# Kernel optimization log

Hardware: AMD Instinct MI355X
Metric: run time of the kernel (lower is better)

Reference implementation:

```python
import jax, jax.numpy as jnp
import numpy as np

N = 8192      # nodes
D_IN = 128    # input features
D_H = 48      # GAT hidden (hardcoded in module)
D_OUT = 32    # control output dim
NEG_INF = -9e15  # matches torch code's -9000000000000000.0


def setup_inputs() -> dict:
    key = jax.random.key(0)
    ks = jax.random.split(key, 12)
    s = 0.05
    return {
        "x": jax.random.normal(ks[0], (N, D_IN), jnp.float32),
        "adj": jax.random.randint(ks[1], (N, N), 0, 2, jnp.int32),
        "W_gat": jax.random.normal(ks[2], (D_H, D_IN), jnp.float32) * s,
        "a": jax.random.normal(ks[3], (1, D_H), jnp.float32) * s,
        "gamma": jnp.ones((D_H,), jnp.float32),
        "beta": jnp.zeros((D_H,), jnp.float32),
        "W1": jax.random.normal(ks[4], (256, D_H), jnp.float32) * s,
        "b1": jnp.zeros((256,), jnp.float32),
        "W2": jax.random.normal(ks[5], (128, 256), jnp.float32) * s,
        "b2": jnp.zeros((128,), jnp.float32),
        "W3": jax.random.normal(ks[6], (D_OUT, 128), jnp.float32) * s,
        "b3": jnp.zeros((D_OUT,), jnp.float32),
    }


def reference(x, adj, W_gat, a, gamma, beta, W1, b1, W2, b2, W3, b3):
    # --- LightweightGATLayer ---
    Wh = x @ W_gat.T                      # [N, D_H]
    s = Wh @ a.T                          # [N, 1] additive attention scores
    e = s + s.T                           # [N, N]
    e = jnp.where(e > 0, e, 0.2 * e)      # LeakyReLU(0.2)
    e = jnp.where(adj > 0, e, NEG_INF)    # mask non-edges
    attn = jax.nn.softmax(e, axis=1)      # row softmax; dropout is identity in eval
    h_prime = attn @ Wh                   # [N, D_H]
    # LayerNorm over last dim, eps=1e-5
    mu = jnp.mean(h_prime, axis=-1, keepdims=True)
    var = jnp.var(h_prime, axis=-1, keepdims=True)
    h = (h_prime - mu) * jax.lax.rsqrt(var + 1e-5) * gamma + beta
    # --- BiACT MLP head: 48 -> 256 -> 128 -> D_OUT ---
    h = jax.nn.relu(h @ W1.T + b1)
    h = jax.nn.relu(h @ W2.T + b2)
    return h @ W3.T + b3                  # [N, D_OUT]
```

## Files before the change

### kernel.cpp

```cpp
#include <hip/hip_runtime.h>

#define N 8192
#define DIN 128
#define DH 48
#define MT 256
#define KC 64
#define PSTR (KC + 8)
#define NSPLIT 16
#define JSPAN (N / NSPLIT)
#define NCHUNK (JSPAN / KC)
#define ACC_STRIDE 64
#define RB 32

typedef _Float16 half8 __attribute__((ext_vector_type(8)));
typedef float f32x4 __attribute__((ext_vector_type(4)));

__global__ __launch_bounds__(256) void k_wh(const float* __restrict__ x,
                                            const float* __restrict__ Wg,
                                            float* __restrict__ Wh) {
    __shared__ float wT[DIN * DH];
    int t = threadIdx.x;
    for (int e = t; e < DIN * DH; e += 256) {
        int c = e / DIN, k = e % DIN;
        wT[k * DH + c] = Wg[e];
    }
    __syncthreads();
    int o = blockIdx.x * 256 + t;
    int r = o / DH, c = o % DH;
    const float4* xr = (const float4*)(x + (size_t)r * DIN);
    float acc = 0.f;
    #pragma unroll 8
    for (int k4 = 0; k4 < DIN / 4; ++k4) {
        float4 xv = xr[k4];
        int kb = k4 * 4;
        acc += xv.x * wT[(kb + 0) * DH + c];
        acc += xv.y * wT[(kb + 1) * DH + c];
        acc += xv.z * wT[(kb + 2) * DH + c];
        acc += xv.w * wT[(kb + 3) * DH + c];
    }
    Wh[o] = acc;
}

__global__ __launch_bounds__(256) void k_s(const float* __restrict__ Wh,
                                           const float* __restrict__ a,
                                           float* __restrict__ s) {
    int r = blockIdx.x * 256 + threadIdx.x;
    const float4* wr = (const float4*)(Wh + (size_t)r * DH);
    const float4* av = (const float4*)a;
    float acc = 0.f;
    #pragma unroll
    for (int k4 = 0; k4 < DH / 4; ++k4) {
        float4 w = wr[k4]; float4 aa = av[k4];
        acc += w.x * aa.x + w.y * aa.y + w.z * aa.z + w.w * aa.w;
    }
    s[r] = acc;
}

__global__ __launch_bounds__(256) void k_gat(const int* __restrict__ adj,
                                             const float* __restrict__ Wh,
                                             const float* __restrict__ s,
                                             float* __restrict__ accWs) {
    __shared__ _Float16 pS[MT][PSTR];
    __shared__ _Float16 wS[64][PSTR];
    __shared__ float sRow[MT];
    int t = threadIdx.x;
    int tile = blockIdx.x & 31;
    int split = blockIdx.x >> 5;
    int i0 = tile * MT;
    int jbase = split * JSPAN;

    sRow[t] = s[i0 + t];
    for (int e = t; e < 16 * PSTR; e += 256) {
        int n = 48 + e / PSTR, k = e % PSTR;
        wS[n][k] = (n == 48) ? (_Float16)1.0f : (_Float16)0.0f;
    }

    int lane = t & 63, w = t >> 6;
    int ln16 = lane & 15, kq = lane >> 4;
    int jp = t & 31, rg = t >> 5;

    f32x4 acc[4][4];
    #pragma unroll
    for (int a0 = 0; a0 < 4; ++a0)
        #pragma unroll
        for (int b0 = 0; b0 < 4; ++b0) acc[a0][b0] = (f32x4){0.f, 0.f, 0.f, 0.f};

    __syncthreads();

    for (int chunk = 0; chunk < NCHUNK; ++chunk) {
        int j0 = jbase + chunk * KC;
        #pragma unroll
        for (int k = 0; k < 12; ++k) {
            int e = t + k * 256;
            int jc = e / DH, d = e % DH;
            wS[d][jc] = (_Float16)Wh[(size_t)j0 * DH + e];
        }
        {
            float2 sj = *(const float2*)(s + j0 + 2 * jp);
            #pragma unroll 8
            for (int it = 0; it < 32; ++it) {
                int r = rg * 32 + it;
                int2 av = *(const int2*)(adj + (size_t)(i0 + r) * N + j0 + 2 * jp);
                float e0 = sRow[r] + sj.x;
                float e1 = sRow[r] + sj.y;
                e0 = fmaxf(e0, 0.2f * e0);
                e1 = fmaxf(e1, 0.2f * e1);
                float p0 = av.x ? __expf(e0) : 0.f;
                float p1 = av.y ? __expf(e1) : 0.f;
                union { _Float16 h[2]; unsigned u; } pk;
                pk.h[0] = (_Float16)p0;
                pk.h[1] = (_Float16)p1;
                *(unsigned*)&pS[r][2 * jp] = pk.u;
            }
        }
        __syncthreads();
        {
            const int m0 = w * 64;
            #pragma unroll
            for (int kt = 0; kt < 2; ++kt) {
                const int kk = kt * 32 + kq * 8;
                half8 b[4];
                #pragma unroll
                for (int nt = 0; nt < 4; ++nt)
                    b[nt] = *(const half8*)&wS[nt * 16 + ln16][kk];
                #pragma unroll
                for (int mtl = 0; mtl < 4; ++mtl) {
                    half8 a = *(const half8*)&pS[m0 + mtl * 16 + ln16][kk];
                    #pragma unroll
                    for (int nt = 0; nt < 4; ++nt)
                        acc[mtl][nt] = __builtin_amdgcn_mfma_f32_16x16x32_f16(
                            a, b[nt], acc[mtl][nt], 0, 0, 0);
                }
            }
        }
        __syncthreads();
    }
    size_t rbase = (size_t)split * N + i0;
    #pragma unroll
    for (int mtl = 0; mtl < 4; ++mtl) {
        #pragma unroll
        for (int nt = 0; nt < 4; ++nt) {
            int col = nt * 16 + ln16;
            if (nt == 3 && ln16 != 0) continue;
            #pragma unroll
            for (int reg = 0; reg < 4; ++reg) {
                int row = w * 64 + mtl * 16 + kq * 4 + reg;
                accWs[(rbase + row) * ACC_STRIDE + col] = acc[mtl][nt][reg];
            }
        }
    }
}

__global__ __launch_bounds__(256) void k_mlp(const float* __restrict__ accWs,
                                             const float* __restrict__ gamma,
                                             const float* __restrict__ beta,
                                             const float* __restrict__ W1, const float* __restrict__ b1,
                                             const float* __restrict__ W2, const float* __restrict__ b2,
                                             const float* __restrict__ W3, const float* __restrict__ b3,
                                             float* __restrict__ out) {
    __shared__ float hacc[RB * 49];
    __shared__ float hN[RB * DH];
    __shared__ float h1[RB * 256];
    __shared__ float h2[RB * 128];
    int t = threadIdx.x;
    int r0 = blockIdx.x * RB;

    for (int e = t; e < RB * 49; e += 256) {
        int r = e / 49, d = e % 49;
        size_t base = (size_t)(r0 + r) * ACC_STRIDE + d;
        float v = 0.f;
        #pragma unroll
        for (int sp = 0; sp < NSPLIT; ++sp)
            v += accWs[(size_t)sp * N * ACC_STRIDE + base];
        hacc[r * 49 + d] = v;
    }
    __syncthreads();

    if (t < RB) {
        float invl = 1.f / hacc[t * 49 + 48];
        float sum = 0.f;
        for (int d = 0; d < DH; ++d) sum += hacc[t * 49 + d];
        float mean = sum * invl * (1.f / DH);
        float var = 0.f;
        for (int d = 0; d < DH; ++d) {
            float dv = hacc[t * 49 + d] * invl - mean;
            var += dv * dv;
        }
        var *= (1.f / DH);
        float rs = rsqrtf(var + 1e-5f);
        for (int d = 0; d < DH; ++d) {
            float hv = (hacc[t * 49 + d] * invl - mean) * rs;
            hN[t * DH + d] = hv * gamma[d] + beta[d];
        }
    }
    __syncthreads();

    {
        int c = t;
        float4 wreg[12];
        const float4* wrow = (const float4*)(W1 + c * DH);
        #pragma unroll
        for (int k4 = 0; k4 < 12; ++k4) wreg[k4] = wrow[k4];
        float bias = b1[c];
        for (int r = 0; r < RB; ++r) {
            float acc = bias;
            const float4* hv4 = (const float4*)&hN[r * DH];
            #pragma unroll
            for (int k4 = 0; k4 < 12; ++k4) {
                float4 hv = hv4[k4];
                acc += hv.x * wreg[k4].x + hv.y * wreg[k4].y
                     + hv.z * wreg[k4].z + hv.w * wreg[k4].w;
            }
            h1[r * 256 + c] = fmaxf(acc, 0.f);
        }
    }
    __syncthreads();

    {
        int c = t & 127;
        int g = t >> 7;
        int rb = g * 16;
        float acc[16];
        float bias = b2[c];
        #pragma unroll
        for (int r = 0; r < 16; ++r) acc[r] = bias;
        const float4* wrow = (const float4*)(W2 + c * 256);
        for (int k4 = 0; k4 < 64; ++k4) {
            float4 wv = wrow[k4];
            #pragma unroll
            for (int r = 0; r < 16; ++r) {
                const float4 hv = *(const float4*)(&h1[(rb + r) * 256 + k4 * 4]);
                acc[r] += wv.x * hv.x + wv.y * hv.y + wv.z * hv.z + wv.w * hv.w;
            }
        }
        #pragma unroll
        for (int r = 0; r < 16; ++r)
            h2[(rb + r) * 128 + c] = fmaxf(acc[r], 0.f);
    }
    __syncthreads();

    {
        int c = t & 31;
        int g = t >> 5;
        int rb = g * 4;
        float acc[4];
        float bias = b3[c];
        #pragma unroll
        for (int r = 0; r < 4; ++r) acc[r] = bias;
        const float4* wrow = (const float4*)(W3 + c * 128);
        for (int k4 = 0; k4 < 32; ++k4) {
            float4 wv = wrow[k4];
            #pragma unroll
            for (int r = 0; r < 4; ++r) {
                const float4 hv = *(const float4*)(&h2[(rb + r) * 128 + k4 * 4]);
                acc[r] += wv.x * hv.x + wv.y * hv.y + wv.z * hv.z + wv.w * hv.w;
            }
        }
        #pragma unroll
        for (int r = 0; r < 4; ++r)
            out[(size_t)(r0 + rb + r) * 32 + c] = acc[r];
    }
}

extern "C" void kernel_launch(void* const* d_in, const int* in_sizes, int n_in,
                              void* d_out, int out_size, void* d_ws, size_t ws_size,
                              hipStream_t stream) {
    const float* x     = (const float*)d_in[0];
    const int*   adj   = (const int*)d_in[1];
    const float* Wg    = (const float*)d_in[2];
    const float* a     = (const float*)d_in[3];
    const float* gamma = (const float*)d_in[4];
    const float* beta  = (const float*)d_in[5];
    const float* W1    = (const float*)d_in[6];
    const float* b1    = (const float*)d_in[7];
    const float* W2    = (const float*)d_in[8];
    const float* b2    = (const float*)d_in[9];
    const float* W3    = (const float*)d_in[10];
    const float* b3    = (const float*)d_in[11];
    float* out = (float*)d_out;

    float* ws = (float*)d_ws;
    float* Wh    = ws;
    float* s     = ws + (size_t)N * DH;
    float* accWs = s + N;

    k_wh<<<N * DH / 256, 256, 0, stream>>>(x, Wg, Wh);
    k_s<<<N / 256, 256, 0, stream>>>(Wh, a, s);
    k_gat<<<32 * NSPLIT, 256, 0, stream>>>(adj, Wh, s, accWs);
    k_mlp<<<N / RB, 256, 0, stream>>>(accWs, gamma, beta, W1, b1, W2, b2, W3, b3, out);
}
```

Before: 465.4 us.

## Register-prefetch adjacency and Wh in GAT kernel, retile, and MFMA-ize MLP layers

The GAT kernel now preloads the next chunk's adjacency and Wh values into registers while the current chunk's MFMA runs, so global loads overlap with compute. The row tile shrinks to 128 and the split count to 8, which keeps 512 blocks but with fewer rows per block. The MLP's first two layers switch from scalar FP32 dot products to f16 MFMA with padded shared-memory strides. This adds register pressure and lowers MLP precision to half.

```diff
diff --git a/kernel.cpp b/kernel.cpp
--- a/kernel.cpp
+++ b/kernel.cpp
@@ -3,10 +3,10 @@
 #define N 8192
 #define DIN 128
 #define DH 48
-#define MT 256
+#define MT 128
 #define KC 64
 #define PSTR (KC + 8)
-#define NSPLIT 16
+#define NSPLIT 8
 #define JSPAN (N / NSPLIT)
 #define NCHUNK (JSPAN / KC)
 #define ACC_STRIDE 64
@@ -64,24 +64,35 @@
     __shared__ _Float16 wS[64][PSTR];
     __shared__ float sRow[MT];
     int t = threadIdx.x;
-    int tile = blockIdx.x & 31;
-    int split = blockIdx.x >> 5;
+    int tile = blockIdx.x & 63;
+    int split = blockIdx.x >> 6;
     int i0 = tile * MT;
     int jbase = split * JSPAN;
 
-    sRow[t] = s[i0 + t];
+    int lane = t & 63, w = t >> 6;
+    int ln16 = lane & 15, kq = lane >> 4;
+    int jp = t & 31, rg = t >> 5;
+
+    const int* adjBase = adj + (size_t)(i0 + rg * 16) * N + jbase + 2 * jp;
+
+    int2 adjR[16];
+    float whR[12];
+    #pragma unroll
+    for (int it = 0; it < 16; ++it)
+        adjR[it] = *(const int2*)(adjBase + (size_t)it * N);
+    #pragma unroll
+    for (int k = 0; k < 12; ++k)
+        whR[k] = Wh[(size_t)jbase * DH + t + k * 256];
+
+    if (t < MT) sRow[t] = s[i0 + t];
     for (int e = t; e < 16 * PSTR; e += 256) {
         int n = 48 + e / PSTR, k = e % PSTR;
         wS[n][k] = (n == 48) ? (_Float16)1.0f : (_Float16)0.0f;
     }
 
-    int lane = t & 63, w = t >> 6;
-    int ln16 = lane & 15, kq = lane >> 4;
-    int jp = t & 31, rg = t >> 5;
-
-    f32x4 acc[4][4];
-    #pragma unroll
-    for (int a0 = 0; a0 < 4; ++a0)
+    f32x4 acc[2][4];
+    #pragma unroll
+    for (int a0 = 0; a0 < 2; ++a0)
         #pragma unroll
         for (int b0 = 0; b0 < 4; ++b0) acc[a0][b0] = (f32x4){0.f, 0.f, 0.f, 0.f};
 
@@ -93,14 +104,14 @@
         for (int k = 0; k < 12; ++k) {
             int e = t + k * 256;
             int jc = e / DH, d = e % DH;
-            wS[d][jc] = (_Float16)Wh[(size_t)j0 * DH + e];
+            wS[d][jc] = (_Float16)whR[k];
         }
         {
             float2 sj = *(const float2*)(s + j0 + 2 * jp);
-            #pragma unroll 8
-            for (int it = 0; it < 32; ++it) {
-                int r = rg * 32 + it;
-                int2 av = *(const int2*)(adj + (size_t)(i0 + r) * N + j0 + 2 * jp);
+            #pragma unroll
+            for (int it = 0; it < 16; ++it) {
+                int r = rg * 16 + it;
+                int2 av = adjR[it];
                 float e0 = sRow[r] + sj.x;
                 float e1 = sRow[r] + sj.y;
                 e0 = fmaxf(e0, 0.2f * e0);
@@ -113,9 +124,18 @@
                 *(unsigned*)&pS[r][2 * jp] = pk.u;
             }
         }
+        if (chunk < NCHUNK - 1) {
+            int jn = j0 + KC;
+            #pragma unroll
+            for (int it = 0; it < 16; ++it)
+                adjR[it] = *(const int2*)(adjBase + (size_t)it * N + (chunk + 1) * KC);
+            #pragma unroll
+            for (int k = 0; k < 12; ++k)
+                whR[k] = Wh[(size_t)jn * DH + t + k * 256];
+        }
         __syncthreads();
         {
-            const int m0 = w * 64;
+            const int m0 = w * 32;
             #pragma unroll
             for (int kt = 0; kt < 2; ++kt) {
                 const int kk = kt * 32 + kq * 8;
@@ -124,7 +144,7 @@
                 for (int nt = 0; nt < 4; ++nt)
                     b[nt] = *(const half8*)&wS[nt * 16 + ln16][kk];
                 #pragma unroll
-                for (int mtl = 0; mtl < 4; ++mtl) {
+                for (int mtl = 0; mtl < 2; ++mtl) {
                     half8 a = *(const half8*)&pS[m0 + mtl * 16 + ln16][kk];
                     #pragma unroll
                     for (int nt = 0; nt < 4; ++nt)
@@ -137,14 +157,14 @@
     }
     size_t rbase = (size_t)split * N + i0;
     #pragma unroll
-    for (int mtl = 0; mtl < 4; ++mtl) {
+    for (int mtl = 0; mtl < 2; ++mtl) {
         #pragma unroll
         for (int nt = 0; nt < 4; ++nt) {
             int col = nt * 16 + ln16;
             if (nt == 3 && ln16 != 0) continue;
             #pragma unroll
             for (int reg = 0; reg < 4; ++reg) {
-                int row = w * 64 + mtl * 16 + kq * 4 + reg;
+                int row = w * 32 + mtl * 16 + kq * 4 + reg;
                 accWs[(rbase + row) * ACC_STRIDE + col] = acc[mtl][nt][reg];
             }
         }
@@ -159,11 +179,13 @@
                                              const float* __restrict__ W3, const float* __restrict__ b3,
                                              float* __restrict__ out) {
     __shared__ float hacc[RB * 49];
-    __shared__ float hN[RB * DH];
-    __shared__ float h1[RB * 256];
-    __shared__ float h2[RB * 128];
+    __shared__ _Float16 hN[RB * 72];
+    __shared__ _Float16 h1[RB * 264];
+    __shared__ float h2[RB * 132];
     int t = threadIdx.x;
     int r0 = blockIdx.x * RB;
+    int lane = t & 63, w = t >> 6;
+    int ln16 = lane & 15, kq = lane >> 4;
 
     for (int e = t; e < RB * 49; e += 256) {
         int r = e / 49, d = e % 49;
@@ -172,7 +194,7 @@
         #pragma unroll
         for (int sp = 0; sp < NSPLIT; ++sp)
             v += accWs[(size_t)sp * N * ACC_STRIDE + base];
-        hacc[r * 49 + d] = v;
+        hacc[e] = v;
     }
     __syncthreads();
 
@@ -190,52 +212,102 @@
         float rs = rsqrtf(var + 1e-5f);
         for (int d = 0; d < DH; ++d) {
             float hv = (hacc[t * 49 + d] * invl - mean) * rs;
-            hN[t * DH + d] = hv * gamma[d] + beta[d];
-        }
+            hN[t * 72 + d] = (_Float16)(hv * gamma[d] + beta[d]);
+        }
+        for (int d = DH; d < 72; ++d) hN[t * 72 + d] = (_Float16)0.f;
     }
     __syncthreads();
 
     {
-        int c = t;
-        float4 wreg[12];
-        const float4* wrow = (const float4*)(W1 + c * DH);
-        #pragma unroll
-        for (int k4 = 0; k4 < 12; ++k4) wreg[k4] = wrow[k4];
-        float bias = b1[c];
-        for (int r = 0; r < RB; ++r) {
-            float acc = bias;
-            const float4* hv4 = (const float4*)&hN[r * DH];
-            #pragma unroll
-            for (int k4 = 0; k4 < 12; ++k4) {
-                float4 hv = hv4[k4];
-                acc += hv.x * wreg[k4].x + hv.y * wreg[k4].y
-                     + hv.z * wreg[k4].z + hv.w * wreg[k4].w;
-            }
-            h1[r * 256 + c] = fmaxf(acc, 0.f);
-        }
+        f32x4 acc1[2][4];
+        #pragma unroll
+        for (int mt = 0; mt < 2; ++mt)
+            #pragma unroll
+            for (int nt = 0; nt < 4; ++nt) acc1[mt][nt] = (f32x4){0.f, 0.f, 0.f, 0.f};
+        #pragma unroll
+        for (int kt = 0; kt < 2; ++kt) {
+            int k = kt * 32 + kq * 8;
+            half8 a[2];
+            #pragma unroll
+            for (int mt = 0; mt < 2; ++mt)
+                a[mt] = *(const half8*)&hN[(mt * 16 + ln16) * 72 + k];
+            #pragma unroll
+            for (int ntl = 0; ntl < 4; ++ntl) {
+                int n = (w * 4 + ntl) * 16 + ln16;
+                half8 b;
+                #pragma unroll
+                for (int i = 0; i < 8; ++i) b[i] = (_Float16)0.f;
+                if (k < DH) {
+                    float4 lo = *(const float4*)(W1 + n * DH + k);
+                    float4 hi = *(const float4*)(W1 + n * DH + k + 4);
+                    b[0] = (_Float16)lo.x; b[1] = (_Float16)lo.y;
+                    b[2] = (_Float16)lo.z; b[3] = (_Float16)lo.w;
+                    b[4] = (_Float16)hi.x; b[5] = (_Float16)hi.y;
+                    b[6] = (_Float16)hi.z; b[7] = (_Float16)hi.w;
+                }
+                #pragma unroll
+                for (int mt = 0; mt < 2; ++mt)
+                    acc1[mt][ntl] = __builtin_amdgcn_mfma_f32_16x16x32_f16(
+                        a[mt], b, acc1[mt][ntl], 0, 0, 0);
+            }
+        }
+        #pragma unroll
+        for (int mt = 0; mt < 2; ++mt)
+            #pragma unroll
+            for (int ntl = 0; ntl < 4; ++ntl) {
+                int col = (w * 4 + ntl) * 16 + ln16;
+                float bias = b1[col];
+                #pragma unroll
+                for (int reg = 0; reg < 4; ++reg) {
+                    int row = mt * 16 + kq * 4 + reg;
+                    float v = acc1[mt][ntl][reg] + bias;
+                    h1[row * 264 + col] = (_Float16)fmaxf(v, 0.f);
+                }
+            }
     }
     __syncthreads();
 
     {
-        int c = t & 127;
-        int g = t >> 7;
-        int rb = g * 16;
-        float acc[16];
-        float bias = b2[c];
-        #pragma unroll
-        for (int r = 0; r < 16; ++r) acc[r] = bias;
-        const float4* wrow = (const float4*)(W2 + c * 256);
-        for (int k4 = 0; k4 < 64; ++k4) {
-            float4 wv = wrow[k4];
-            #pragma unroll
-            for (int r = 0; r < 16; ++r) {
-                const float4 hv = *(const float4*)(&h1[(rb + r) * 256 + k4 * 4]);
-                acc[r] += wv.x * hv.x + wv.y * hv.y + wv.z * hv.z + wv.w * hv.w;
-            }
-        }
-        #pragma unroll
-        for (int r = 0; r < 16; ++r)
-            h2[(rb + r) * 128 + c] = fmaxf(acc[r], 0.f);
+        f32x4 acc2[2][2];
+        #pragma unroll
+        for (int mt = 0; mt < 2; ++mt)
+            #pragma unroll
+            for (int nt = 0; nt < 2; ++nt) acc2[mt][nt] = (f32x4){0.f, 0.f, 0.f, 0.f};
+        #pragma unroll
+        for (int kt = 0; kt < 8; ++kt) {
+            int k = kt * 32 + kq * 8;
+            half8 a[2];
+            #pragma unroll
+            for (int mt = 0; mt < 2; ++mt)
+                a[mt] = *(const half8*)&h1[(mt * 16 + ln16) * 264 + k];
+            #pragma unroll
+            for (int ntl = 0; ntl < 2; ++ntl) {
+                int n = (w * 2 + ntl) * 16 + ln16;
+                float4 lo = *(const float4*)(W2 + n * 256 + k);
+                float4 hi = *(const float4*)(W2 + n * 256 + k + 4);
+                half8 b;
+                b[0] = (_Float16)lo.x; b[1] = (_Float16)lo.y;
+                b[2] = (_Float16)lo.z; b[3] = (_Float16)lo.w;
+                b[4] = (_Float16)hi.x; b[5] = (_Float16)hi.y;
+                b[6] = (_Float16)hi.z; b[7] = (_Float16)hi.w;
+                #pragma unroll
+                for (int mt = 0; mt < 2; ++mt)
+                    acc2[mt][ntl] = __builtin_amdgcn_mfma_f32_16x16x32_f16(
+                        a[mt], b, acc2[mt][ntl], 0, 0, 0);
+            }
+        }
+        #pragma unroll
+        for (int mt = 0; mt < 2; ++mt)
+            #pragma unroll
+            for (int ntl = 0; ntl < 2; ++ntl) {
+                int col = (w * 2 + ntl) * 16 + ln16;
+                float bias = b2[col];
+                #pragma unroll
+                for (int reg = 0; reg < 4; ++reg) {
+                    int row = mt * 16 + kq * 4 + reg;
+                    h2[row * 132 + col] = fmaxf(acc2[mt][ntl][reg] + bias, 0.f);
+                }
+            }
     }
     __syncthreads();
 
@@ -252,7 +324,7 @@
             float4 wv = wrow[k4];
             #pragma unroll
             for (int r = 0; r < 4; ++r) {
-                const float4 hv = *(const float4*)(&h2[(rb + r) * 128 + k4 * 4]);
+                const float4 hv = *(const float4*)(&h2[(rb + r) * 132 + k4 * 4]);
                 acc[r] += wv.x * hv.x + wv.y * hv.y + wv.z * hv.z + wv.w * hv.w;
             }
         }
@@ -286,6 +358,6 @@
 
     k_wh<<<N * DH / 256, 256, 0, stream>>>(x, Wg, Wh);
     k_s<<<N / 256, 256, 0, stream>>>(Wh, a, s);
-    k_gat<<<32 * NSPLIT, 256, 0, stream>>>(adj, Wh, s, accWs);
+    k_gat<<<64 * NSPLIT, 256, 0, stream>>>(adj, Wh, s, accWs);
     k_mlp<<<N / RB, 256, 0, stream>>>(accWs, gamma, beta, W1, b1, W2, b2, W3, b3, out);
 }
```

Result: no change. 467.0 us (+0.4%).
